# Kernel tuning notes

Hardware: AMD Instinct MI355X
Metric: run time of the kernel (lower is better)

Reference implementation:

```python
import jax, jax.numpy as jnp
import numpy as np

B, T, D, E, FF, K = 4, 1024, 1024, 8, 2048, 2
SINKHORN_ITERS = 3


def setup_inputs() -> dict:
    key = jax.random.key(0)
    ks = jax.random.split(key, 7)
    scale = 0.02
    return {
        "x": jax.random.normal(ks[0], (B, T, D), dtype=jnp.float32),
        "router_w": jax.random.normal(ks[1], (E, D), dtype=jnp.float32) * scale,  # nn.Linear(D,E).weight
        "router_b": jnp.zeros((E,), dtype=jnp.float32),
        "temperature": jnp.ones((1,), dtype=jnp.float32) * 0.5,
        "wg": jax.random.normal(ks[2], (E, D, FF), dtype=jnp.float32) * scale,   # expert gate weights
        "wp": jax.random.normal(ks[3], (E, D, FF), dtype=jnp.float32) * scale,   # expert proj weights
        "wo": jax.random.normal(ks[4], (E, FF, D), dtype=jnp.float32) * scale,   # expert out_proj weights
    }


def _sinkhorn(log_alpha, iters=SINKHORN_ITERS):
    for _ in range(iters):
        log_alpha = log_alpha - jax.nn.logsumexp(log_alpha, axis=-1, keepdims=True)
        log_alpha = log_alpha - jax.nn.logsumexp(log_alpha, axis=-2, keepdims=True)
    gates = jnp.exp(log_alpha)
    return gates / (jnp.sum(gates, axis=-1, keepdims=True) + 1e-8)


def reference(x, router_w, router_b, temperature, wg, wp, wo):
    # Router scores with clamped temperature (clamp(min=0.1))
    temp = jnp.maximum(temperature, 0.1)
    scores = (jnp.einsum("btd,ed->bte", x, router_w) + router_b) / temp  # [B,T,E]

    # T>1 and E>1 -> Sinkhorn doubly-stochastic normalization
    gates = _sinkhorn(scores)

    topk_vals, topk_idx = jax.lax.top_k(gates, K)                 # [B,T,K]
    topk_gates = topk_vals / (jnp.sum(topk_vals, axis=-1, keepdims=True) + 1e-8)

    # Dense all-expert FFN (relu-gated GLU), matching mask-and-sum semantics.
    # sum_k sum_i (idx_k==i)*gate_k*expert_i(x) == sum_k gate_k * expert_{idx_k}(x)
    g = jax.nn.relu(jnp.einsum("btd,edf->btef", x, wg))           # [B,T,E,FF]
    p = jnp.einsum("btd,edf->btef", x, wp)                        # [B,T,E,FF]
    all_out = jnp.einsum("btef,efd->bted", g * p, wo)             # [B,T,E,D]

    gathered = jnp.take_along_axis(all_out, topk_idx[..., None], axis=2)  # [B,T,K,D]
    expert_out = jnp.sum(gathered * topk_gates[..., None], axis=2)        # [B,T,D]

    return x + expert_out
```

## Files before the change

kernel.cpp:

```cpp
#include <hip/hip_runtime.h>
#include <hip/hip_bf16.h>
#include <stdint.h>

#define B_   4
#define T_   1024
#define D_   1024
#define E_   8
#define FF_  2048
#define NT_  4096
#define LCAP 9472
#define NTS1 (D_ / 64)
#define NTS2 (FF_ / 64)

typedef unsigned short u16;
typedef __attribute__((ext_vector_type(8))) short bf16x8;
typedef __attribute__((ext_vector_type(4))) float f32x4;

#define MFMA16(a, b, c) __builtin_amdgcn_mfma_f32_16x16x32_bf16((a), (b), (c), 0, 0, 0)

__device__ __forceinline__ u16 f2bf(float f) {
  union { float f; uint32_t u; } c; c.f = f;
  return (u16)((c.u + 0x7FFFu + ((c.u >> 16) & 1u)) >> 16);
}

__device__ __forceinline__ void gl_lds16(const void* g, void* l) {
  __builtin_amdgcn_global_load_lds(
      (const __attribute__((address_space(1))) uint32_t*)g,
      (__attribute__((address_space(3))) uint32_t*)l, 16, 0, 0);
}


__global__ __launch_bounds__(256) void k_router(const float* __restrict__ x,
                                                const float* __restrict__ rw,
                                                const float* __restrict__ rb,
                                                const float* __restrict__ temp,
                                                float* __restrict__ scores,
                                                float* __restrict__ out,
                                                u16* __restrict__ xb,
                                                int* __restrict__ tok, float* __restrict__ gate,
                                                int* __restrict__ cnt, int* __restrict__ cur) {
  const int gid = blockIdx.x * 256 + threadIdx.x;
  if (gid < LCAP) { tok[gid] = 0; gate[gid] = 0.f; }
  if (gid < E_)   { cnt[gid] = 0; cur[gid] = 0; }

  int wid  = gid >> 6;
  int lane = threadIdx.x & 63;
  const float* xr = x + (size_t)wid * D_;
  float* orow = out + (size_t)wid * D_;
  u16* xrow = xb + (size_t)wid * D_;
  float acc[E_];
  #pragma unroll
  for (int e = 0; e < E_; ++e) acc[e] = 0.f;
  for (int i = lane; i < D_; i += 64) {
    float xv = xr[i];
    orow[i] = xv;
    xrow[i] = f2bf(xv);
    #pragma unroll
    for (int e = 0; e < E_; ++e) acc[e] += xv * rw[e * D_ + i];
  }
  float inv = 1.0f / fmaxf(temp[0], 0.1f);
  #pragma unroll
  for (int e = 0; e < E_; ++e) {
    float v = acc[e];
    for (int off = 32; off; off >>= 1) v += __shfl_xor(v, off);
    if (lane == 0) scores[(size_t)wid * E_ + e] = (v + rb[e]) * inv;
  }
}

__global__ __launch_bounds__(1024) void k_sinkhorn(const float* __restrict__ scores,
                                                   float* __restrict__ tkg, int* __restrict__ tki,
                                                   int* __restrict__ cnt) {
  const int b = blockIdx.x, t = threadIdx.x;
  const int row = b * T_ + t;
  float s[E_];
  #pragma unroll
  for (int e = 0; e < E_; ++e) s[e] = scores[(size_t)row * E_ + e];

  __shared__ float red[16][E_];
  __shared__ float redv[E_];
  __shared__ int lcnt[E_];
  if (t < E_) lcnt[t] = 0;
  const int wid = t >> 6, lane = t & 63;

  for (int it = 0; it < 3; ++it) {
    float m = s[0];
    #pragma unroll
    for (int e = 1; e < E_; ++e) m = fmaxf(m, s[e]);
    float sum = 0.f;
    #pragma unroll
    for (int e = 0; e < E_; ++e) sum += expf(s[e] - m);
    float lse = m + logf(sum);
    #pragma unroll
    for (int e = 0; e < E_; ++e) s[e] -= lse;

    #pragma unroll
    for (int e = 0; e < E_; ++e) {
      float v = s[e];
      for (int off = 32; off; off >>= 1) v = fmaxf(v, __shfl_xor(v, off));
      if (lane == 0) red[wid][e] = v;
    }
    __syncthreads();
    if (t < E_) {
      float mm = red[0][t];
      #pragma unroll
      for (int wv = 1; wv < 16; ++wv) mm = fmaxf(mm, red[wv][t]);
      redv[t] = mm;
    }
    __syncthreads();
    float cm[E_];
    #pragma unroll
    for (int e = 0; e < E_; ++e) cm[e] = redv[e];

    #pragma unroll
    for (int e = 0; e < E_; ++e) {
      float v = expf(s[e] - cm[e]);
      for (int off = 32; off; off >>= 1) v += __shfl_xor(v, off);
      if (lane == 0) red[wid][e] = v;
    }
    __syncthreads();
    if (t < E_) {
      float ss = 0.f;
      #pragma unroll
      for (int wv = 0; wv < 16; ++wv) ss += red[wv][t];
      redv[t] = ss;
    }
    __syncthreads();
    #pragma unroll
    for (int e = 0; e < E_; ++e) s[e] -= cm[e] + logf(redv[e]);
    __syncthreads();
  }

  float g[E_]; float rs = 0.f;
  #pragma unroll
  for (int e = 0; e < E_; ++e) { g[e] = expf(s[e]); rs += g[e]; }
  float inv = 1.f / (rs + 1e-8f);
  #pragma unroll
  for (int e = 0; e < E_; ++e) g[e] *= inv;

  int i0 = 0; float v0 = g[0];
  #pragma unroll
  for (int e = 1; e < E_; ++e) if (g[e] > v0) { v0 = g[e]; i0 = e; }
  int i1 = -1; float v1 = -1e30f;
  #pragma unroll
  for (int e = 0; e < E_; ++e) if (e != i0 && g[e] > v1) { v1 = g[e]; i1 = e; }
  float den = 1.f / (v0 + v1 + 1e-8f);
  tkg[row * 2 + 0] = v0 * den; tki[row * 2 + 0] = i0;
  tkg[row * 2 + 1] = v1 * den; tki[row * 2 + 1] = i1;

  atomicAdd(&lcnt[i0], 1);
  atomicAdd(&lcnt[i1], 1);
  __syncthreads();
  if (t < E_) atomicAdd(&cnt[t], lcnt[t]);
}

__global__ void k_offsets(const int* __restrict__ cnt, int* __restrict__ segoff) {
  if (threadIdx.x == 0 && blockIdx.x == 0) {
    int run = 0;
    for (int e = 0; e < E_; ++e) { segoff[e] = run; run += ((cnt[e] + 127) >> 7) << 7; }
    segoff[E_] = run;
  }
}

__global__ __launch_bounds__(256) void k_scatter(const int* __restrict__ tki, const float* __restrict__ tkg,
                                                 const int* __restrict__ segoff, int* __restrict__ cur,
                                                 int* __restrict__ tok, float* __restrict__ gate) {
  int idx = blockIdx.x * 256 + threadIdx.x;
  int row = idx >> 1;
  int e = tki[idx];
  float g = tkg[idx];
  int pos = atomicAdd(&cur[e], 1);
  int p = segoff[e] + pos;
  tok[p] = row;
  gate[p] = g;
}


__global__ __launch_bounds__(256) void k_transpose_wgp(const float* __restrict__ wg,
                                                       const float* __restrict__ wp,
                                                       u16* __restrict__ wa) {
  __shared__ __align__(16) u16 ldsT[128][136];
  const int e = blockIdx.z >> 1, iswp = blockIdx.z & 1;
  const float* src = (iswp ? wp : wg) + (size_t)e * D_ * FF_;
  const int woff = iswp * 16;
  const int f0 = blockIdx.x * 128, d0 = blockIdx.y * 128;
  const int tid = threadIdx.x;
  #pragma unroll
  for (int it = 0; it < 16; ++it) {
    const int fi = it * 256 + tid;
    const int rowd = fi >> 5;
    const int col4 = fi & 31;
    const float4 v = *(const float4*)(src + (size_t)(d0 + rowd) * FF_ + f0 + col4 * 4);
    ldsT[col4 * 4 + 0][rowd] = f2bf(v.x);
    ldsT[col4 * 4 + 1][rowd] = f2bf(v.y);
    ldsT[col4 * 4 + 2][rowd] = f2bf(v.z);
    ldsT[col4 * 4 + 3][rowd] = f2bf(v.w);
  }
  __syncthreads();
  const int cl = tid >> 1, half = tid & 1;
  const int f = f0 + cl;
  const int fp = ((f >> 4) << 5) + (f & 15) + woff;
  u16* dst = wa + (size_t)e * 4096 * 1024 + (size_t)fp * 1024 + d0 + half * 64;
  const u16* srcl = &ldsT[cl][half * 64];
  #pragma unroll
  for (int i = 0; i < 8; ++i)
    *(uint4*)(dst + i * 8) = *(const uint4*)(srcl + i * 8);
}

__global__ __launch_bounds__(256) void k_transpose_wo(const float* __restrict__ wo,
                                                      u16* __restrict__ woT) {
  __shared__ __align__(16) u16 ldsT[128][136];
  const int e = blockIdx.z;
  const float* src = wo + (size_t)e * FF_ * D_;
  const int d0 = blockIdx.x * 128, ff0 = blockIdx.y * 128;
  const int tid = threadIdx.x;
  #pragma unroll
  for (int it = 0; it < 16; ++it) {
    const int fi = it * 256 + tid;
    const int rowf = fi >> 5;
    const int col4 = fi & 31;
    const float4 v = *(const float4*)(src + (size_t)(ff0 + rowf) * D_ + d0 + col4 * 4);
    ldsT[col4 * 4 + 0][rowf] = f2bf(v.x);
    ldsT[col4 * 4 + 1][rowf] = f2bf(v.y);
    ldsT[col4 * 4 + 2][rowf] = f2bf(v.z);
    ldsT[col4 * 4 + 3][rowf] = f2bf(v.w);
  }
  __syncthreads();
  const int dl = tid >> 1, half = tid & 1;
  u16* dst = woT + (size_t)e * D_ * FF_ + (size_t)(d0 + dl) * FF_ + ff0 + half * 64;
  const u16* srcl = &ldsT[dl][half * 64];
  #pragma unroll
  for (int i = 0; i < 8; ++i)
    *(uint4*)(dst + i * 8) = *(const uint4*)(srcl + i * 8);
}


__global__ __launch_bounds__(512, 2) void k_stage1(
    const u16* __restrict__ wa, const u16* __restrict__ xb,
    const int* __restrict__ tok, const int* __restrict__ segoff,
    u16* __restrict__ H) {
  const int raw = blockIdx.x;
  const int e   = raw & 7;
  const int rem = raw >> 3;
  const int ft  = rem >> 4;
  const int pt2 = rem & 15;
  const int seg0 = segoff[e], segend = segoff[e + 1];
  if (pt2 * 256 >= segend - seg0) return;
  const int tid = threadIdx.x;
  const int lane = tid & 63;
  const int w = tid >> 6;
  const int lane15 = lane & 15, lchunk = lane >> 4;
  const int lk8 = lchunk * 8;
  const int fw = w >> 2, pw = w & 3;

  __shared__ __align__(16) u16 LA[2][16384];
  __shared__ __align__(16) u16 LB[2][16384];

  const int prow0 = seg0 + pt2 * 256;
  const u16* asrc0 = wa + (size_t)e * 4096 * 1024
                        + (size_t)(ft * 256 + 2 * w * 16 + lane15) * 1024 + lk8;
  const u16* asrc1 = asrc0 + 16 * 1024;
  const int tk0 = tok[prow0 + 2 * w * 16 + lane15];
  const int tk1 = tok[prow0 + 2 * w * 16 + 16 + lane15];
  const u16* bsrc0 = xb + (size_t)tk0 * D_ + lk8;
  const u16* bsrc1 = xb + (size_t)tk1 * D_ + lk8;
  const int dA0 = 2 * w * 512, dA1 = dA0 + 512;

  const f32x4 vz = {0.f, 0.f, 0.f, 0.f};
  f32x4 acc[8][4];
  #pragma unroll
  for (int m = 0; m < 8; ++m)
    #pragma unroll
    for (int n = 0; n < 4; ++n) acc[m][n] = vz;

#define STG_A(c, s) do { const int o_ = (s) * 64;           \
    gl_lds16(asrc0 + o_,      &LA[c][dA0]);                 \
    gl_lds16(asrc0 + o_ + 32, &LA[c][dA0 + 8192]);          \
    gl_lds16(asrc1 + o_,      &LA[c][dA1]);                 \
    gl_lds16(asrc1 + o_ + 32, &LA[c][dA1 + 8192]); } while (0)
#define STG_B(c, s) do { const int o_ = (s) * 64;           \
    gl_lds16(bsrc0 + o_,      &LB[c][dA0]);                 \
    gl_lds16(bsrc0 + o_ + 32, &LB[c][dA0 + 8192]);          \
    gl_lds16(bsrc1 + o_,      &LB[c][dA1]);                 \
    gl_lds16(bsrc1 + o_ + 32, &LB[c][dA1 + 8192]); } while (0)

  STG_A(0, 0); STG_B(0, 0);
  #pragma unroll 1
  for (int s = 0; s < NTS1; ++s) {
    const int c = s & 1;
    asm volatile("s_waitcnt vmcnt(0)" ::: "memory");
    __builtin_amdgcn_s_barrier();
    asm volatile("" ::: "memory");
    const u16* la = LA[c];
    const u16* lb = LB[c];
    bf16x8 bv[4][2];
    #pragma unroll
    for (int n = 0; n < 4; ++n)
      #pragma unroll
      for (int kc = 0; kc < 2; ++kc)
        bv[n][kc] = *(const bf16x8*)(lb + kc * 8192 + (pw * 4 + n) * 512 + lane * 8);
    #pragma unroll
    for (int p = 0; p < 4; ++p) {
      bf16x8 av[2][2];
      #pragma unroll
      for (int mm = 0; mm < 2; ++mm)
        #pragma unroll
        for (int kc = 0; kc < 2; ++kc)
          av[mm][kc] = *(const bf16x8*)(la + kc * 8192 + (fw * 8 + 2 * p + mm) * 512 + lane * 8);
      if (p == 0) { if (s + 1 < NTS1) STG_A(c ^ 1, s + 1); }
      if (p == 1) { if (s + 1 < NTS1) STG_B(c ^ 1, s + 1); }
      __builtin_amdgcn_s_setprio(1);
      #pragma unroll
      for (int mm = 0; mm < 2; ++mm)
        #pragma unroll
        for (int n = 0; n < 4; ++n)
          #pragma unroll
          for (int kc = 0; kc < 2; ++kc)
            acc[2 * p + mm][n] = MFMA16(av[mm][kc], bv[n][kc], acc[2 * p + mm][n]);
      __builtin_amdgcn_s_setprio(0);
      if (p < 3) {
        __builtin_amdgcn_s_barrier();
        asm volatile("" ::: "memory");
      }
    }
  }
#undef STG_A
#undef STG_B

  const int jrow = lchunk * 4;
  #pragma unroll
  for (int q = 0; q < 4; ++q) {
    const int fcol = ft * 128 + fw * 64 + q * 16 + jrow;
    #pragma unroll
    for (int n = 0; n < 4; ++n) {
      const int prow = prow0 + pw * 64 + n * 16 + lane15;
      if (prow < segend) {
        union { uint2 v; u16 s[4]; } u;
        #pragma unroll
        for (int j = 0; j < 4; ++j)
          u.s[j] = f2bf(fmaxf(acc[2 * q][n][j], 0.f) * acc[2 * q + 1][n][j]);
        *(uint2*)(H + (size_t)prow * FF_ + fcol) = u.v;
      }
    }
  }
}

__global__ __launch_bounds__(512, 2) void k_stage2(
    const u16* __restrict__ H, const u16* __restrict__ woT,
    const int* __restrict__ tok, const float* __restrict__ gate,
    const int* __restrict__ cnt, const int* __restrict__ segoff,
    float* __restrict__ out) {
  const int raw = blockIdx.x;
  const int dt  = raw & 7;
  const int rem = raw >> 3;
  const int e   = rem >> 5;
  const int pt  = rem & 31;
  if (pt * 128 >= cnt[e]) return;
  const int tid = threadIdx.x;
  const int lane = tid & 63;
  const int w = tid >> 6;
  const int lane15 = lane & 15, lchunk = lane >> 4;
  const int lk8 = lchunk * 8;
  const int ph = w >> 2, dq = w & 3;

  __shared__ __align__(16) u16 LH[2][8192];
  __shared__ __align__(16) u16 LW[2][8192];
  __shared__ int   ltok[128];
  __shared__ float lgt[128];

  const int prow0 = segoff[e] + pt * 128;
  if (tid < 128) { ltok[tid] = tok[prow0 + tid]; lgt[tid] = gate[prow0 + tid]; }

  const u16* hsrc = H + (size_t)(prow0 + w * 16 + lane15) * FF_ + lk8;
  const u16* wsrc = woT + (size_t)e * D_ * FF_
                        + (size_t)(dt * 128 + w * 16 + lane15) * FF_ + lk8;
  const int dstb = w * 512;

  const f32x4 vz = {0.f, 0.f, 0.f, 0.f};
  f32x4 acc[4][2];
  #pragma unroll
  for (int m = 0; m < 4; ++m)
    #pragma unroll
    for (int n = 0; n < 2; ++n) acc[m][n] = vz;

#define STG_H(c, s) do { const int o_ = (s) * 64;           \
    gl_lds16(hsrc + o_,      &LH[c][dstb]);                 \
    gl_lds16(hsrc + o_ + 32, &LH[c][dstb + 4096]); } while (0)
#define STG_W(c, s) do { const int o_ = (s) * 64;           \
    gl_lds16(wsrc + o_,      &LW[c][dstb]);                 \
    gl_lds16(wsrc + o_ + 32, &LW[c][dstb + 4096]); } while (0)

  STG_H(0, 0); STG_W(0, 0);
  #pragma unroll 1
  for (int s = 0; s < NTS2; ++s) {
    const int c = s & 1;
    asm volatile("s_waitcnt vmcnt(0)" ::: "memory");
    __builtin_amdgcn_s_barrier();
    asm volatile("" ::: "memory");
    const u16* lh = LH[c];
    const u16* lw = LW[c];
    bf16x8 bw[2][2];
    #pragma unroll
    for (int n = 0; n < 2; ++n)
      #pragma unroll
      for (int kc = 0; kc < 2; ++kc)
        bw[n][kc] = *(const bf16x8*)(lw + kc * 4096 + (dq * 2 + n) * 512 + lane * 8);
    #pragma unroll
    for (int p = 0; p < 2; ++p) {
      bf16x8 ah[2][2];
      #pragma unroll
      for (int mm = 0; mm < 2; ++mm)
        #pragma unroll
        for (int kc = 0; kc < 2; ++kc)
          ah[mm][kc] = *(const bf16x8*)(lh + kc * 4096 + (ph * 4 + 2 * p + mm) * 512 + lane * 8);
      if (p == 0) { if (s + 1 < NTS2) STG_H(c ^ 1, s + 1); }
      if (p == 1) { if (s + 1 < NTS2) STG_W(c ^ 1, s + 1); }
      __builtin_amdgcn_s_setprio(1);
      #pragma unroll
      for (int mm = 0; mm < 2; ++mm)
        #pragma unroll
        for (int n = 0; n < 2; ++n)
          #pragma unroll
          for (int kc = 0; kc < 2; ++kc)
            acc[2 * p + mm][n] = MFMA16(ah[mm][kc], bw[n][kc], acc[2 * p + mm][n]);
      __builtin_amdgcn_s_setprio(0);
      if (p == 0) {
        __builtin_amdgcn_s_barrier();
        asm volatile("" ::: "memory");
      }
    }
  }
#undef STG_H
#undef STG_W

  const int jrow = lchunk * 4;
  #pragma unroll
  for (int m = 0; m < 4; ++m) {
    #pragma unroll
    for (int n = 0; n < 2; ++n) {
      const int dcol = dt * 128 + dq * 32 + n * 16 + lane15;
      #pragma unroll
      for (int j = 0; j < 4; ++j) {
        const int pl = ph * 64 + m * 16 + jrow + j;
        unsafeAtomicAdd(&out[(size_t)ltok[pl] * D_ + dcol], lgt[pl] * acc[m][n][j]);
      }
    }
  }
}


extern "C" void kernel_launch(void* const* d_in, const int* in_sizes, int n_in,
                              void* d_out, int out_size, void* d_ws, size_t ws_size,
                              hipStream_t stream) {
  const float* x    = (const float*)d_in[0];
  const float* rw   = (const float*)d_in[1];
  const float* rb   = (const float*)d_in[2];
  const float* temp = (const float*)d_in[3];
  const float* wg   = (const float*)d_in[4];
  const float* wp   = (const float*)d_in[5];
  const float* wo   = (const float*)d_in[6];
  float* out = (float*)d_out;
  char* ws = (char*)d_ws;

  const size_t O_XB  = 0;
  const size_t O_WA  = 8388608;
  const size_t O_WOT = O_WA;
  const size_t O_H   = O_WA + 67108864;
  const size_t O_SC  = O_H + (size_t)LCAP * FF_ * 2;
  const size_t O_TKG = O_SC + (size_t)NT_ * E_ * 4;
  const size_t O_TKI = O_TKG + (size_t)NT_ * 2 * 4;
  const size_t O_CNT = O_TKI + (size_t)NT_ * 2 * 4;
  const size_t O_CUR = O_CNT + 128;
  const size_t O_SEG = O_CUR + 128;
  const size_t O_TOK = O_SEG + 128;
  const size_t O_GTE = O_TOK + (size_t)LCAP * 4;
  const size_t REQ   = O_GTE + (size_t)LCAP * 4;
  if (ws_size < REQ) return;

  u16*   xb     = (u16*)(ws + O_XB);
  u16*   wa     = (u16*)(ws + O_WA);
  u16*   woT    = (u16*)(ws + O_WOT);
  u16*   Hbuf   = (u16*)(ws + O_H);
  float* scores = (float*)(ws + O_SC);
  float* tkg    = (float*)(ws + O_TKG);
  int*   tki    = (int*)(ws + O_TKI);
  int*   cnt    = (int*)(ws + O_CNT);
  int*   cur    = (int*)(ws + O_CUR);
  int*   segoff = (int*)(ws + O_SEG);
  int*   tok    = (int*)(ws + O_TOK);
  float* gate   = (float*)(ws + O_GTE);

  k_router<<<NT_ / 4, 256, 0, stream>>>(x, rw, rb, temp, scores, out, xb,
                                        tok, gate, cnt, cur);
  k_sinkhorn<<<B_, 1024, 0, stream>>>(scores, tkg, tki, cnt);
  k_offsets<<<1, 64, 0, stream>>>(cnt, segoff);
  k_scatter<<<(NT_ * 2) / 256, 256, 0, stream>>>(tki, tkg, segoff, cur, tok, gate);

  k_transpose_wgp<<<dim3(FF_ / 128, D_ / 128, E_ * 2), 256, 0, stream>>>(wg, wp, wa);

  k_stage1<<<16 * 16 * E_, 512, 0, stream>>>(wa, xb, tok, segoff, Hbuf);

  k_transpose_wo<<<dim3(D_ / 128, FF_ / 128, E_), 256, 0, stream>>>(wo, woT);

  k_stage2<<<32 * 8 * E_, 512, 0, stream>>>(Hbuf, woT, tok, gate, cnt, segoff, out);
}
```

Baseline: 431.6 us.

## Switch expert GEMMs to triple-buffered K=32 LDS pipeline with higher occupancy

```diff
diff --git a/kernel.cpp b/kernel.cpp
--- a/kernel.cpp
+++ b/kernel.cpp
@@ -9,8 +9,8 @@
 #define FF_  2048
 #define NT_  4096
 #define LCAP 9472
-#define NTS1 (D_ / 64)
-#define NTS2 (FF_ / 64)
+#define NS1  (D_ / 32)
+#define NS2  (FF_ / 32)
 
 typedef unsigned short u16;
 typedef __attribute__((ext_vector_type(8))) short bf16x8;
@@ -252,8 +252,8 @@
   const int lk8 = lchunk * 8;
   const int fw = w >> 2, pw = w & 3;
 
-  __shared__ __align__(16) u16 LA[2][16384];
-  __shared__ __align__(16) u16 LB[2][16384];
+  __shared__ __align__(16) u16 LA[3][8192];
+  __shared__ __align__(16) u16 LB[3][8192];
 
   const int prow0 = seg0 + pt2 * 256;
   const u16* asrc0 = wa + (size_t)e * 4096 * 1024
@@ -272,50 +272,42 @@
     #pragma unroll
     for (int n = 0; n < 4; ++n) acc[m][n] = vz;
 
-#define STG_A(c, s) do { const int o_ = (s) * 64;           \
-    gl_lds16(asrc0 + o_,      &LA[c][dA0]);                 \
-    gl_lds16(asrc0 + o_ + 32, &LA[c][dA0 + 8192]);          \
-    gl_lds16(asrc1 + o_,      &LA[c][dA1]);                 \
-    gl_lds16(asrc1 + o_ + 32, &LA[c][dA1 + 8192]); } while (0)
-#define STG_B(c, s) do { const int o_ = (s) * 64;           \
-    gl_lds16(bsrc0 + o_,      &LB[c][dA0]);                 \
-    gl_lds16(bsrc0 + o_ + 32, &LB[c][dA0 + 8192]);          \
-    gl_lds16(bsrc1 + o_,      &LB[c][dA1]);                 \
-    gl_lds16(bsrc1 + o_ + 32, &LB[c][dA1 + 8192]); } while (0)
+#define STG_A(c, s) do { const int o_ = (s) * 32;           \
+    gl_lds16(asrc0 + o_, &LA[c][dA0]);                      \
+    gl_lds16(asrc1 + o_, &LA[c][dA1]); } while (0)
+#define STG_B(c, s) do { const int o_ = (s) * 32;           \
+    gl_lds16(bsrc0 + o_, &LB[c][dA0]);                      \
+    gl_lds16(bsrc1 + o_, &LB[c][dA1]); } while (0)
 
   STG_A(0, 0); STG_B(0, 0);
+  STG_A(1, 1); STG_B(1, 1);
   #pragma unroll 1
-  for (int s = 0; s < NTS1; ++s) {
-    const int c = s & 1;
-    asm volatile("s_waitcnt vmcnt(0)" ::: "memory");
+  for (int s = 0; s < NS1; ++s) {
+    const int c = s % 3;
+    if (s < NS1 - 1) asm volatile("s_waitcnt vmcnt(4)" ::: "memory");
+    else             asm volatile("s_waitcnt vmcnt(0)" ::: "memory");
     __builtin_amdgcn_s_barrier();
     asm volatile("" ::: "memory");
     const u16* la = LA[c];
     const u16* lb = LB[c];
-    bf16x8 bv[4][2];
+    bf16x8 bv[4];
     #pragma unroll
     for (int n = 0; n < 4; ++n)
-      #pragma unroll
-      for (int kc = 0; kc < 2; ++kc)
-        bv[n][kc] = *(const bf16x8*)(lb + kc * 8192 + (pw * 4 + n) * 512 + lane * 8);
+      bv[n] = *(const bf16x8*)(lb + (pw * 4 + n) * 512 + lane * 8);
     #pragma unroll
     for (int p = 0; p < 4; ++p) {
-      bf16x8 av[2][2];
+      bf16x8 av[2];
       #pragma unroll
       for (int mm = 0; mm < 2; ++mm)
-        #pragma unroll
-        for (int kc = 0; kc < 2; ++kc)
-          av[mm][kc] = *(const bf16x8*)(la + kc * 8192 + (fw * 8 + 2 * p + mm) * 512 + lane * 8);
-      if (p == 0) { if (s + 1 < NTS1) STG_A(c ^ 1, s + 1); }
-      if (p == 1) { if (s + 1 < NTS1) STG_B(c ^ 1, s + 1); }
+        av[mm] = *(const bf16x8*)(la + (fw * 8 + 2 * p + mm) * 512 + lane * 8);
+      if (p == 0) { if (s + 2 < NS1) STG_A((s + 2) % 3, s + 2); }
+      if (p == 1) { if (s + 2 < NS1) STG_B((s + 2) % 3, s + 2); }
       __builtin_amdgcn_s_setprio(1);
       #pragma unroll
       for (int mm = 0; mm < 2; ++mm)
         #pragma unroll
         for (int n = 0; n < 4; ++n)
-          #pragma unroll
-          for (int kc = 0; kc < 2; ++kc)
-            acc[2 * p + mm][n] = MFMA16(av[mm][kc], bv[n][kc], acc[2 * p + mm][n]);
+          acc[2 * p + mm][n] = MFMA16(av[mm], bv[n], acc[2 * p + mm][n]);
       __builtin_amdgcn_s_setprio(0);
       if (p < 3) {
         __builtin_amdgcn_s_barrier();
@@ -344,7 +336,7 @@
   }
 }
 
-__global__ __launch_bounds__(512, 2) void k_stage2(
+__global__ __launch_bounds__(512, 4) void k_stage2(
     const u16* __restrict__ H, const u16* __restrict__ woT,
     const int* __restrict__ tok, const float* __restrict__ gate,
     const int* __restrict__ cnt, const int* __restrict__ segoff,
@@ -362,14 +354,10 @@
   const int lk8 = lchunk * 8;
   const int ph = w >> 2, dq = w & 3;
 
-  __shared__ __align__(16) u16 LH[2][8192];
-  __shared__ __align__(16) u16 LW[2][8192];
-  __shared__ int   ltok[128];
-  __shared__ float lgt[128];
+  __shared__ __align__(16) u16 LH[3][4096];
+  __shared__ __align__(16) u16 LW[3][4096];
 
   const int prow0 = segoff[e] + pt * 128;
-  if (tid < 128) { ltok[tid] = tok[prow0 + tid]; lgt[tid] = gate[prow0 + tid]; }
-
   const u16* hsrc = H + (size_t)(prow0 + w * 16 + lane15) * FF_ + lk8;
   const u16* wsrc = woT + (size_t)e * D_ * FF_
                         + (size_t)(dt * 128 + w * 16 + lane15) * FF_ + lk8;
@@ -382,46 +370,38 @@
     #pragma unroll
     for (int n = 0; n < 2; ++n) acc[m][n] = vz;
 
-#define STG_H(c, s) do { const int o_ = (s) * 64;           \
-    gl_lds16(hsrc + o_,      &LH[c][dstb]);                 \
-    gl_lds16(hsrc + o_ + 32, &LH[c][dstb + 4096]); } while (0)
-#define STG_W(c, s) do { const int o_ = (s) * 64;           \
-    gl_lds16(wsrc + o_,      &LW[c][dstb]);                 \
-    gl_lds16(wsrc + o_ + 32, &LW[c][dstb + 4096]); } while (0)
+#define STG_H(c, s) gl_lds16(hsrc + (s) * 32, &LH[c][dstb])
+#define STG_W(c, s) gl_lds16(wsrc + (s) * 32, &LW[c][dstb])
 
   STG_H(0, 0); STG_W(0, 0);
+  STG_H(1, 1); STG_W(1, 1);
   #pragma unroll 1
-  for (int s = 0; s < NTS2; ++s) {
-    const int c = s & 1;
-    asm volatile("s_waitcnt vmcnt(0)" ::: "memory");
+  for (int s = 0; s < NS2; ++s) {
+    const int c = s % 3;
+    if (s < NS2 - 1) asm volatile("s_waitcnt vmcnt(2)" ::: "memory");
+    else             asm volatile("s_waitcnt vmcnt(0)" ::: "memory");
     __builtin_amdgcn_s_barrier();
     asm volatile("" ::: "memory");
     const u16* lh = LH[c];
     const u16* lw = LW[c];
-    bf16x8 bw[2][2];
+    bf16x8 bw[2];
     #pragma unroll
     for (int n = 0; n < 2; ++n)
-      #pragma unroll
-      for (int kc = 0; kc < 2; ++kc)
-        bw[n][kc] = *(const bf16x8*)(lw + kc * 4096 + (dq * 2 + n) * 512 + lane * 8);
+      bw[n] = *(const bf16x8*)(lw + (dq * 2 + n) * 512 + lane * 8);
     #pragma unroll
     for (int p = 0; p < 2; ++p) {
-      bf16x8 ah[2][2];
+      bf16x8 ah[2];
       #pragma unroll
       for (int mm = 0; mm < 2; ++mm)
-        #pragma unroll
-        for (int kc = 0; kc < 2; ++kc)
-          ah[mm][kc] = *(const bf16x8*)(lh + kc * 4096 + (ph * 4 + 2 * p + mm) * 512 + lane * 8);
-      if (p == 0) { if (s + 1 < NTS2) STG_H(c ^ 1, s + 1); }
-      if (p == 1) { if (s + 1 < NTS2) STG_W(c ^ 1, s + 1); }
+        ah[mm] = *(const bf16x8*)(lh + (ph * 4 + 2 * p + mm) * 512 + lane * 8);
+      if (p == 0) { if (s + 2 < NS2) STG_H((s + 2) % 3, s + 2); }
+      if (p == 1) { if (s + 2 < NS2) STG_W((s + 2) % 3, s + 2); }
       __builtin_amdgcn_s_setprio(1);
       #pragma unroll
       for (int mm = 0; mm < 2; ++mm)
         #pragma unroll
         for (int n = 0; n < 2; ++n)
-          #pragma unroll
-          for (int kc = 0; kc < 2; ++kc)
-            acc[2 * p + mm][n] = MFMA16(ah[mm][kc], bw[n][kc], acc[2 * p + mm][n]);
+          acc[2 * p + mm][n] = MFMA16(ah[mm], bw[n], acc[2 * p + mm][n]);
       __builtin_amdgcn_s_setprio(0);
       if (p == 0) {
         __builtin_amdgcn_s_barrier();
@@ -436,12 +416,14 @@
   #pragma unroll
   for (int m = 0; m < 4; ++m) {
     #pragma unroll
-    for (int n = 0; n < 2; ++n) {
-      const int dcol = dt * 128 + dq * 32 + n * 16 + lane15;
-      #pragma unroll
-      for (int j = 0; j < 4; ++j) {
-        const int pl = ph * 64 + m * 16 + jrow + j;
-        unsafeAtomicAdd(&out[(size_t)ltok[pl] * D_ + dcol], lgt[pl] * acc[m][n][j]);
+    for (int j = 0; j < 4; ++j) {
+      const int prow = prow0 + ph * 64 + m * 16 + jrow + j;
+      const int tk = tok[prow];
+      const float gt = gate[prow];
+      #pragma unroll
+      for (int n = 0; n < 2; ++n) {
+        const int dcol = dt * 128 + dq * 32 + n * 16 + lane15;
+        unsafeAtomicAdd(&out[(size_t)tk * D_ + dcol], gt * acc[m][n][j]);
       }
     }
   }
```

Result: slower. 454.0 us (+5.2%).
